# Performance work log

Measured on AMD Instinct MI355X. Metric: run time of the kernel, lower is better.

## Reference

```python
import jax, jax.numpy as jnp
import numpy as np

B = 1024          # batch_size from init
TEMP = 0.5        # temperature buffer
EPS_NORM = 1e-12  # F.normalize eps
EPS_COS = 1e-8    # F.cosine_similarity eps


def setup_inputs() -> dict:
    key = jax.random.key(0)
    k1, k2 = jax.random.split(key)
    emb_i = jax.random.normal(k1, (B, 128, 128), dtype=jnp.float32)
    emb_j = jax.random.normal(k2, (B, 128, 128), dtype=jnp.float32)
    return {"emb_i": emb_i, "emb_j": emb_j}


def reference(emb_i, emb_j):
    # F.normalize(x, dim=1): L2-normalize over the m axis of [B, m, n]
    def norm_dim1(x):
        n = jnp.sqrt(jnp.sum(x * x, axis=1, keepdims=True))
        return x / jnp.maximum(n, EPS_NORM)

    z_i = norm_dim1(emb_i)
    z_j = norm_dim1(emb_j)
    reps = jnp.concatenate([z_i, z_j], axis=0)        # [2B, m, n]
    flat = reps.reshape(2 * B, -1)                    # [2B, D]

    # cosine similarity of flattened vectors == matmul of re-normalized rows
    rn = flat / jnp.maximum(
        jnp.sqrt(jnp.sum(flat * flat, axis=1, keepdims=True)), EPS_COS)
    sim = rn @ rn.T                                   # [2B, 2B]

    sim_ij = jnp.diagonal(sim, offset=B)              # [B]
    sim_ji = jnp.diagonal(sim, offset=-B)             # [B]
    positives = jnp.concatenate([sim_ij, sim_ji], axis=0)  # [2B]

    negatives_mask = 1.0 - jnp.eye(2 * B, dtype=sim.dtype)
    nominator = jnp.exp(positives / TEMP)
    denominator = jnp.sum(negatives_mask * jnp.exp(sim / TEMP), axis=1)
    loss_partial = -jnp.log(nominator / denominator)
    return jnp.sum(loss_partial) / (2 * B)
```

## Files before the change

kernel.cpp:

```cpp
#include <hip/hip_runtime.h>
#include <hip/hip_bf16.h>
#include <math.h>

#define B_SZ   1024
#define NROW   2048
#define D_K    16384
#define SPLIT  8
#define KSEG   (D_K / SPLIT)
#define NTILE  16
#define NPAIR  136
#define TEMP_SIM (2.0f / 256.0f)

typedef float f32x4 __attribute__((ext_vector_type(4)));
typedef long  i64;

typedef __attribute__((address_space(1))) unsigned int GU32;
typedef __attribute__((address_space(3))) unsigned int LU32;

__device__ __forceinline__ void async16(const void* g, void* l) {
  __builtin_amdgcn_global_load_lds((GU32*)(g), (LU32*)(l), 16, 0, 0);
}

__global__ __launch_bounds__(512) void norm_kernel(
    const float* __restrict__ emb_i, const float* __restrict__ emb_j,
    unsigned char* __restrict__ rn, float* __restrict__ sim,
    float* __restrict__ rsum, unsigned int* __restrict__ cnt)
{
  const int b = blockIdx.x;
  const int t = threadIdx.x;
  const int c = t & 31;
  const int g = t >> 5;

  ((f32x4*)sim)[(size_t)b * 512 + t] = (f32x4){0.f, 0.f, 0.f, 0.f};
  if (b == 0) {
    for (int k = t; k < NROW; k += 512) rsum[k] = 0.f;
    if (t == 0) *cnt = 0u;
  }

  const float* src = (b < B_SZ) ? (emb_i + (size_t)b * D_K)
                                : (emb_j + (size_t)(b - B_SZ) * D_K);

  f32x4 vals[8];
  f32x4 ss = (f32x4){0.f, 0.f, 0.f, 0.f};
#pragma unroll
  for (int mm = 0; mm < 8; ++mm) {
    f32x4 v = *(const f32x4*)(src + (size_t)(g * 8 + mm) * 128 + c * 4);
    vals[mm] = v;
    ss += v * v;
  }

  __shared__ f32x4 part[16][32];
  part[g][c] = ss;
  __syncthreads();
  f32x4 css = part[0][c];
#pragma unroll
  for (int gg = 1; gg < 16; ++gg) css += part[gg][c];

  f32x4 mcn, colz2;
#pragma unroll
  for (int k = 0; k < 4; ++k) {
    mcn[k] = fmaxf(sqrtf(css[k]), 1e-12f);
    colz2[k] = css[k] / (mcn[k] * mcn[k]);
  }
  float s = colz2[0] + colz2[1] + colz2[2] + colz2[3];
#pragma unroll
  for (int off = 1; off < 64; off <<= 1) s += __shfl_xor(s, off);
  const float rowfac = fmaxf(sqrtf(0.5f * s), 1e-8f);

  f32x4 scale;
#pragma unroll
  for (int k = 0; k < 4; ++k) scale[k] = 16.0f / (mcn[k] * rowfac);

  unsigned char* dst = rn + (size_t)b * D_K;
#pragma unroll
  for (int mm = 0; mm < 8; ++mm) {
    f32x4 sv = vals[mm] * scale;
    int p = 0;
    p = __builtin_amdgcn_cvt_pk_fp8_f32(sv[0], sv[1], p, false);
    p = __builtin_amdgcn_cvt_pk_fp8_f32(sv[2], sv[3], p, true);
    *(int*)(dst + (size_t)(g * 8 + mm) * 128 + c * 4) = p;
  }
}

__global__ __launch_bounds__(256) void gemm_sim_kernel(
    const unsigned char* __restrict__ rn, float* __restrict__ sim)
{
  int idx = blockIdx.y, tI = 0, rem = NTILE;
  while (idx >= rem) { idx -= rem; --rem; ++tI; }
  const int tJ = tI + idx;
  const bool diag = (tI == tJ);

  const int kBase = blockIdx.x * KSEG;
  const int t    = threadIdx.x;
  const int lane = t & 63;
  const int wave = t >> 6;
  const int wm = wave >> 1, wn = wave & 1;
  const int quad = lane >> 4, col = lane & 15;

  __shared__ __align__(16) unsigned char As[128 * 128];
  __shared__ __align__(16) unsigned char Bs[128 * 128];

  const int srow = t >> 3;
  const int gc   = (t & 7) ^ (srow & 7);
  const unsigned char* aGb = rn + (size_t)(tI * 128 + srow) * D_K + kBase + gc * 16;
  const unsigned char* bGb = rn + (size_t)(tJ * 128 + srow) * D_K + kBase + gc * 16;

  f32x4 acc[4][4];
#pragma unroll
  for (int mi = 0; mi < 4; ++mi)
#pragma unroll
    for (int ni = 0; ni < 4; ++ni)
      acc[mi][ni] = (f32x4){0.f, 0.f, 0.f, 0.f};

  for (int k0 = 0; k0 < KSEG; k0 += 128) {
    __syncthreads();
#pragma unroll
    for (int i = 0; i < 4; ++i) {
      async16(aGb + (size_t)(32 * i) * D_K + k0, &As[i * 4096 + t * 16]);
      async16(bGb + (size_t)(32 * i) * D_K + k0, &Bs[i * 4096 + t * 16]);
    }
    __syncthreads();

#pragma unroll
    for (int h = 0; h < 4; ++h) {
      const int off = ((2 * h + (quad >> 1)) ^ (col & 7)) * 16 + (quad & 1) * 8;
      i64 af[4], bf[4];
#pragma unroll
      for (int mi = 0; mi < 4; ++mi)
        af[mi] = *(const i64*)(&As[(wm * 64 + mi * 16 + col) * 128 + off]);
#pragma unroll
      for (int ni = 0; ni < 4; ++ni)
        bf[ni] = *(const i64*)(&Bs[(wn * 64 + ni * 16 + col) * 128 + off]);
#pragma unroll
      for (int mi = 0; mi < 4; ++mi)
#pragma unroll
        for (int ni = 0; ni < 4; ++ni)
          acc[mi][ni] = __builtin_amdgcn_mfma_f32_16x16x32_fp8_fp8(
              af[mi], bf[ni], acc[mi][ni], 0, 0, 0);
    }
  }

  const int iB = tI * 128 + wm * 64;
  const int jB = tJ * 128 + wn * 64;
#pragma unroll
  for (int mi = 0; mi < 4; ++mi) {
#pragma unroll
    for (int reg = 0; reg < 4; ++reg) {
      const int i = iB + mi * 16 + quad * 4 + reg;
#pragma unroll
      for (int ni = 0; ni < 4; ++ni) {
        const int j = jB + ni * 16 + col;
        if (!diag || j >= i)
          atomicAdd(&sim[(size_t)i * NROW + j], acc[mi][ni][reg]);
      }
    }
  }
}

__global__ __launch_bounds__(256) void loss_tile_kernel(
    const float* __restrict__ sim, float* __restrict__ rsum,
    unsigned int* __restrict__ cnt, float* __restrict__ out)
{
  int idx = blockIdx.x, tI = 0, rem = NTILE;
  while (idx >= rem) { idx -= rem; --rem; ++tI; }
  const int tJ = tI + idx;
  const bool diag = (tI == tJ);

  const int t   = threadIdx.x;
  const int w   = t >> 6;
  const int l   = t & 63;
  const int hf  = l >> 5;
  const int sub = l & 31;
  const int jb  = tJ * 128 + sub * 4;

  float ca[4] = {0.f, 0.f, 0.f, 0.f};

#pragma unroll
  for (int step = 0; step < 16; ++step) {
    const int r  = w * 32 + step * 2 + hf;
    const int gi = tI * 128 + r;
    f32x4 v = *(const f32x4*)(sim + (size_t)gi * NROW + jb);
    float e[4];
#pragma unroll
    for (int k = 0; k < 4; ++k) {
      e[k] = __expf(TEMP_SIM * v[k]);
      if (diag && (jb + k <= gi)) e[k] = 0.f;
      ca[k] += e[k];
    }
    float rp = e[0] + e[1] + e[2] + e[3];
#pragma unroll
    for (int off = 1; off < 32; off <<= 1) rp += __shfl_xor(rp, off);
    if (sub == 0) atomicAdd(&rsum[gi], rp);
  }

  __shared__ float colacc[8][128];
#pragma unroll
  for (int k = 0; k < 4; ++k) colacc[w * 2 + hf][sub * 4 + k] = ca[k];
  __syncthreads();
  if (t < 128) {
    float s = 0.f;
#pragma unroll
    for (int q = 0; q < 8; ++q) s += colacc[q][t];
    atomicAdd(&rsum[tJ * 128 + t], s);
  }

  __syncthreads();
  __shared__ bool last;
  if (t == 0) {
    __threadfence();
    last = (atomicAdd(cnt, 1u) == NPAIR - 1);
  }
  __syncthreads();
  if (!last) return;

  float s = 0.f;
  for (int i = t; i < NROW; i += 256) {
    const int jp = (i < B_SZ) ? i + B_SZ : i - B_SZ;
    const float pos = (jp >= i) ? sim[(size_t)i * NROW + jp]
                                : sim[(size_t)jp * NROW + i];
    const float rs = atomicAdd(&rsum[i], 0.f);
    s += logf(rs) - TEMP_SIM * pos;
  }
#pragma unroll
  for (int off = 1; off < 64; off <<= 1) s += __shfl_xor(s, off);
  __shared__ float r[4];
  if ((t & 63) == 0) r[t >> 6] = s;
  __syncthreads();
  if (t == 0) out[0] = (r[0] + r[1] + r[2] + r[3]) * (1.0f / NROW);
}

extern "C" void kernel_launch(void* const* d_in, const int* in_sizes, int n_in,
                              void* d_out, int out_size, void* d_ws, size_t ws_size,
                              hipStream_t stream) {
  const float* emb_i = (const float*)d_in[0];
  const float* emb_j = (const float*)d_in[1];
  float* out = (float*)d_out;

  char* ws = (char*)d_ws;
  unsigned char* rn = (unsigned char*)ws;
  float* sim  = (float*)(ws + (size_t)NROW * D_K);
  float* rsum = sim + (size_t)NROW * NROW;
  unsigned int* cnt = (unsigned int*)(rsum + NROW);

  norm_kernel<<<dim3(NROW), dim3(512), 0, stream>>>(emb_i, emb_j, rn, sim, rsum, cnt);
  gemm_sim_kernel<<<dim3(SPLIT, NPAIR), dim3(256), 0, stream>>>(rn, sim);
  loss_tile_kernel<<<dim3(NPAIR), dim3(256), 0, stream>>>(sim, rsum, cnt, out);
}
```

Baseline: 259.4 us.

## Switch GEMM to 32x32x64 scaled FP8 MFMA and fuse loss into GEMM tail

After: 730.2 us. +181.5%, slower.

```diff
diff --git a/kernel.cpp b/kernel.cpp
--- a/kernel.cpp
+++ b/kernel.cpp
@@ -11,8 +11,10 @@
 #define NPAIR  136
 #define TEMP_SIM (2.0f / 256.0f)
 
-typedef float f32x4 __attribute__((ext_vector_type(4)));
-typedef long  i64;
+typedef float f32x4  __attribute__((ext_vector_type(4)));
+typedef float f32x16 __attribute__((ext_vector_type(16)));
+typedef int   i32x4  __attribute__((ext_vector_type(4)));
+typedef int   i32x8  __attribute__((ext_vector_type(8)));
 
 typedef __attribute__((address_space(1))) unsigned int GU32;
 typedef __attribute__((address_space(3))) unsigned int LU32;
@@ -24,7 +26,8 @@
 __global__ __launch_bounds__(512) void norm_kernel(
     const float* __restrict__ emb_i, const float* __restrict__ emb_j,
     unsigned char* __restrict__ rn, float* __restrict__ sim,
-    float* __restrict__ rsum, unsigned int* __restrict__ cnt)
+    float* __restrict__ rsum, unsigned int* __restrict__ cnt,
+    unsigned int* __restrict__ tileCnt)
 {
   const int b = blockIdx.x;
   const int t = threadIdx.x;
@@ -34,6 +37,7 @@
   ((f32x4*)sim)[(size_t)b * 512 + t] = (f32x4){0.f, 0.f, 0.f, 0.f};
   if (b == 0) {
     for (int k = t; k < NROW; k += 512) rsum[k] = 0.f;
+    for (int k = t; k < NPAIR; k += 512) tileCnt[k] = 0u;
     if (t == 0) *cnt = 0u;
   }
 
@@ -83,9 +87,12 @@
 }
 
 __global__ __launch_bounds__(256) void gemm_sim_kernel(
-    const unsigned char* __restrict__ rn, float* __restrict__ sim)
+    const unsigned char* __restrict__ rn, float* __restrict__ sim,
+    float* __restrict__ rsum, unsigned int* __restrict__ cnt,
+    unsigned int* __restrict__ tileCnt, float* __restrict__ out)
 {
-  int idx = blockIdx.y, tI = 0, rem = NTILE;
+  const int tileIdx = blockIdx.y;
+  int idx = tileIdx, tI = 0, rem = NTILE;
   while (idx >= rem) { idx -= rem; --rem; ++tI; }
   const int tJ = tI + idx;
   const bool diag = (tI == tJ);
@@ -95,7 +102,7 @@
   const int lane = t & 63;
   const int wave = t >> 6;
   const int wm = wave >> 1, wn = wave & 1;
-  const int quad = lane >> 4, col = lane & 15;
+  const int l31 = lane & 31, l5 = lane >> 5;
 
   __shared__ __align__(16) unsigned char As[128 * 128];
   __shared__ __align__(16) unsigned char Bs[128 * 128];
@@ -105,12 +112,12 @@
   const unsigned char* aGb = rn + (size_t)(tI * 128 + srow) * D_K + kBase + gc * 16;
   const unsigned char* bGb = rn + (size_t)(tJ * 128 + srow) * D_K + kBase + gc * 16;
 
-  f32x4 acc[4][4];
-#pragma unroll
-  for (int mi = 0; mi < 4; ++mi)
-#pragma unroll
-    for (int ni = 0; ni < 4; ++ni)
-      acc[mi][ni] = (f32x4){0.f, 0.f, 0.f, 0.f};
+  f32x16 acc[2][2];
+#pragma unroll
+  for (int mi = 0; mi < 2; ++mi)
+#pragma unroll
+    for (int ni = 0; ni < 2; ++ni)
+      acc[mi][ni] = (f32x16)(0.f);
 
   for (int k0 = 0; k0 < KSEG; k0 += 128) {
     __syncthreads();
@@ -122,108 +129,117 @@
     __syncthreads();
 
 #pragma unroll
-    for (int h = 0; h < 4; ++h) {
-      const int off = ((2 * h + (quad >> 1)) ^ (col & 7)) * 16 + (quad & 1) * 8;
-      i64 af[4], bf[4];
-#pragma unroll
-      for (int mi = 0; mi < 4; ++mi)
-        af[mi] = *(const i64*)(&As[(wm * 64 + mi * 16 + col) * 128 + off]);
-#pragma unroll
-      for (int ni = 0; ni < 4; ++ni)
-        bf[ni] = *(const i64*)(&Bs[(wn * 64 + ni * 16 + col) * 128 + off]);
-#pragma unroll
-      for (int mi = 0; mi < 4; ++mi)
-#pragma unroll
-        for (int ni = 0; ni < 4; ++ni)
-          acc[mi][ni] = __builtin_amdgcn_mfma_f32_16x16x32_fp8_fp8(
-              af[mi], bf[ni], acc[mi][ni], 0, 0, 0);
+    for (int s = 0; s < 2; ++s) {
+      const int g = s * 4 + l5 * 2;
+      i32x8 af[2], bf[2];
+#pragma unroll
+      for (int mi = 0; mi < 2; ++mi) {
+        const int row = wm * 64 + mi * 32 + l31;
+        const int r7 = row & 7;
+        i32x4 lo = *(const i32x4*)(&As[row * 128 + (g ^ r7) * 16]);
+        i32x4 hi = *(const i32x4*)(&As[row * 128 + ((g + 1) ^ r7) * 16]);
+        af[mi][0] = lo[0]; af[mi][1] = lo[1]; af[mi][2] = lo[2]; af[mi][3] = lo[3];
+        af[mi][4] = hi[0]; af[mi][5] = hi[1]; af[mi][6] = hi[2]; af[mi][7] = hi[3];
+      }
+#pragma unroll
+      for (int ni = 0; ni < 2; ++ni) {
+        const int row = wn * 64 + ni * 32 + l31;
+        const int r7 = row & 7;
+        i32x4 lo = *(const i32x4*)(&Bs[row * 128 + (g ^ r7) * 16]);
+        i32x4 hi = *(const i32x4*)(&Bs[row * 128 + ((g + 1) ^ r7) * 16]);
+        bf[ni][0] = lo[0]; bf[ni][1] = lo[1]; bf[ni][2] = lo[2]; bf[ni][3] = lo[3];
+        bf[ni][4] = hi[0]; bf[ni][5] = hi[1]; bf[ni][6] = hi[2]; bf[ni][7] = hi[3];
+      }
+#pragma unroll
+      for (int mi = 0; mi < 2; ++mi)
+#pragma unroll
+        for (int ni = 0; ni < 2; ++ni)
+          acc[mi][ni] = __builtin_amdgcn_mfma_scale_f32_32x32x64_f8f6f4(
+              af[mi], bf[ni], acc[mi][ni], 0, 0,
+              0, 0x7F7F7F7F,
+              0, 0x7F7F7F7F);
     }
   }
 
   const int iB = tI * 128 + wm * 64;
   const int jB = tJ * 128 + wn * 64;
 #pragma unroll
-  for (int mi = 0; mi < 4; ++mi) {
-#pragma unroll
-    for (int reg = 0; reg < 4; ++reg) {
-      const int i = iB + mi * 16 + quad * 4 + reg;
-#pragma unroll
-      for (int ni = 0; ni < 4; ++ni) {
-        const int j = jB + ni * 16 + col;
+  for (int mi = 0; mi < 2; ++mi) {
+#pragma unroll
+    for (int ni = 0; ni < 2; ++ni) {
+#pragma unroll
+      for (int reg = 0; reg < 16; ++reg) {
+        const int i = iB + mi * 32 + (reg & 3) + 8 * (reg >> 2) + 4 * l5;
+        const int j = jB + ni * 32 + l31;
         if (!diag || j >= i)
           atomicAdd(&sim[(size_t)i * NROW + j], acc[mi][ni][reg]);
       }
     }
   }
-}
-
-__global__ __launch_bounds__(256) void loss_tile_kernel(
-    const float* __restrict__ sim, float* __restrict__ rsum,
-    unsigned int* __restrict__ cnt, float* __restrict__ out)
-{
-  int idx = blockIdx.x, tI = 0, rem = NTILE;
-  while (idx >= rem) { idx -= rem; --rem; ++tI; }
-  const int tJ = tI + idx;
-  const bool diag = (tI == tJ);
-
-  const int t   = threadIdx.x;
-  const int w   = t >> 6;
-  const int l   = t & 63;
-  const int hf  = l >> 5;
-  const int sub = l & 31;
-  const int jb  = tJ * 128 + sub * 4;
-
-  float ca[4] = {0.f, 0.f, 0.f, 0.f};
-
-#pragma unroll
-  for (int step = 0; step < 16; ++step) {
-    const int r  = w * 32 + step * 2 + hf;
-    const int gi = tI * 128 + r;
-    f32x4 v = *(const f32x4*)(sim + (size_t)gi * NROW + jb);
-    float e[4];
-#pragma unroll
-    for (int k = 0; k < 4; ++k) {
-      e[k] = __expf(TEMP_SIM * v[k]);
-      if (diag && (jb + k <= gi)) e[k] = 0.f;
-      ca[k] += e[k];
-    }
-    float rp = e[0] + e[1] + e[2] + e[3];
-#pragma unroll
-    for (int off = 1; off < 32; off <<= 1) rp += __shfl_xor(rp, off);
-    if (sub == 0) atomicAdd(&rsum[gi], rp);
-  }
-
-  __shared__ float colacc[8][128];
-#pragma unroll
-  for (int k = 0; k < 4; ++k) colacc[w * 2 + hf][sub * 4 + k] = ca[k];
-  __syncthreads();
-  if (t < 128) {
-    float s = 0.f;
-#pragma unroll
-    for (int q = 0; q < 8; ++q) s += colacc[q][t];
-    atomicAdd(&rsum[tJ * 128 + t], s);
-  }
-
-  __syncthreads();
-  __shared__ bool last;
-  if (t == 0) {
-    __threadfence();
-    last = (atomicAdd(cnt, 1u) == NPAIR - 1);
-  }
-  __syncthreads();
-  if (!last) return;
+
+  __threadfence();
+  __syncthreads();
+  int* flag = (int*)Bs;
+  if (t == 0) flag[8] = (atomicAdd(&tileCnt[tileIdx], 1u) == SPLIT - 1);
+  __syncthreads();
+  if (!flag[8]) return;
+
+  {
+    const int w   = t >> 6;
+    const int l   = t & 63;
+    const int hf  = l >> 5;
+    const int sub = l & 31;
+    const int jb  = tJ * 128 + sub * 4;
+    float* colacc = (float*)As;
+
+    float ca[4] = {0.f, 0.f, 0.f, 0.f};
+#pragma unroll
+    for (int step = 0; step < 16; ++step) {
+      const int r  = w * 32 + step * 2 + hf;
+      const int gi = tI * 128 + r;
+      float* base = &sim[(size_t)gi * NROW + jb];
+      float e[4];
+#pragma unroll
+      for (int k = 0; k < 4; ++k) {
+        const float v = atomicAdd(&base[k], 0.f);
+        float ev = __expf(TEMP_SIM * v);
+        if (diag && (jb + k <= gi)) ev = 0.f;
+        e[k] = ev;
+        ca[k] += ev;
+      }
+      float rp = e[0] + e[1] + e[2] + e[3];
+#pragma unroll
+      for (int off = 1; off < 32; off <<= 1) rp += __shfl_xor(rp, off);
+      if (sub == 0) atomicAdd(&rsum[gi], rp);
+    }
+#pragma unroll
+    for (int k = 0; k < 4; ++k) colacc[(w * 2 + hf) * 128 + sub * 4 + k] = ca[k];
+    __syncthreads();
+    if (t < 128) {
+      float s = 0.f;
+#pragma unroll
+      for (int q = 0; q < 8; ++q) s += colacc[q * 128 + t];
+      atomicAdd(&rsum[tJ * 128 + t], s);
+    }
+  }
+
+  __threadfence();
+  __syncthreads();
+  if (t == 0) flag[8] = (atomicAdd(cnt, 1u) == NPAIR - 1);
+  __syncthreads();
+  if (!flag[8]) return;
 
   float s = 0.f;
   for (int i = t; i < NROW; i += 256) {
     const int jp = (i < B_SZ) ? i + B_SZ : i - B_SZ;
-    const float pos = (jp >= i) ? sim[(size_t)i * NROW + jp]
-                                : sim[(size_t)jp * NROW + i];
-    const float rs = atomicAdd(&rsum[i], 0.f);
+    float* pp = (jp >= i) ? &sim[(size_t)i * NROW + jp] : &sim[(size_t)jp * NROW + i];
+    const float pos = atomicAdd(pp, 0.f);
+    const float rs  = atomicAdd(&rsum[i], 0.f);
     s += logf(rs) - TEMP_SIM * pos;
   }
 #pragma unroll
   for (int off = 1; off < 64; off <<= 1) s += __shfl_xor(s, off);
-  __shared__ float r[4];
+  float* r = (float*)As;
   if ((t & 63) == 0) r[t >> 6] = s;
   __syncthreads();
   if (t == 0) out[0] = (r[0] + r[1] + r[2] + r[3]) * (1.0f / NROW);
@@ -241,8 +257,10 @@
   float* sim  = (float*)(ws + (size_t)NROW * D_K);
   float* rsum = sim + (size_t)NROW * NROW;
   unsigned int* cnt = (unsigned int*)(rsum + NROW);
-
-  norm_kernel<<<dim3(NROW), dim3(512), 0, stream>>>(emb_i, emb_j, rn, sim, rsum, cnt);
-  gemm_sim_kernel<<<dim3(SPLIT, NPAIR), dim3(256), 0, stream>>>(rn, sim);
-  loss_tile_kernel<<<dim3(NPAIR), dim3(256), 0, stream>>>(sim, rsum, cnt, out);
-}
+  unsigned int* tileCnt = cnt + 1;
+
+  norm_kernel<<<dim3(NROW), dim3(512), 0, stream>>>(emb_i, emb_j, rn, sim,
+                                                    rsum, cnt, tileCnt);
+  gemm_sim_kernel<<<dim3(SPLIT, NPAIR), dim3(256), 0, stream>>>(
+      rn, sim, rsum, cnt, tileCnt, out);
+}
```
